# Optimization experiments

Measured on AMD Instinct MI355X. Metric: run time of the kernel, lower is better.

Reference implementation:

```python
import jax, jax.numpy as jnp
import numpy as np

N0, N1, N2 = 100000, 200000, 100000
DEG = 8
D = 128
NC = 16
NHE = 20000
HE_TOT = 200000

def spmm(rows, cols, vals, x, n):
    # y = A @ x for COO sparse A (n x m); x: [m, d] -> [n, d]
    return jax.ops.segment_sum(vals[:, None] * x[cols], rows, num_segments=n)

def setup_inputs():
    key = jax.random.key(0)
    ks = iter(jax.random.split(key, 64))
    def randn(shape, scale=1.0):
        return jax.random.normal(next(ks), shape, dtype=jnp.float32) * scale
    def ridx(n, hi):
        return jax.random.randint(next(ks), (n,), 0, hi, dtype=jnp.int32)
    inp = {}
    inp['X0'] = randn((N0, D)); inp['X1'] = randn((N1, D)); inp['X2'] = randn((N2, D))
    for i, n in [(0, N0), (1, N1), (2, N2)]:
        nnz = DEG * n
        for tag in ['L', 'Lu', 'Ld']:
            inp[f'{tag}{i}'] = jnp.stack([ridx(nnz, n), ridx(nnz, n)])
            inp[f'{tag}{i}v'] = randn((nnz,), 0.1)
    inp['B1r'] = ridx(2 * N1, N0); inp['B1c'] = ridx(2 * N1, N1); inp['B1v'] = randn((2 * N1,), 0.1)
    inp['B2r'] = ridx(3 * N2, N1); inp['B2c'] = ridx(3 * N2, N2); inp['B2v'] = randn((3 * N2,), 0.1)
    inp['he_idx'] = ridx(HE_TOT, N0)
    inp['he_seg'] = jnp.sort(ridx(HE_TOT, NHE))
    inp['W'] = randn((3, 3, 6, D, D), 0.05)  # [layer, simplex-dim, term, in, out]
    inp['Wfc'] = randn((D, D), 0.05)
    inp['Wcls'] = randn((D, NC), 0.05)
    inp['bcls'] = jnp.zeros((NC,), jnp.float32)
    return inp

def reference(X0, X1, X2, L0, L0v, Lu0, Lu0v, Ld0, Ld0v, L1, L1v, Lu1, Lu1v, Ld1, Ld1v, L2, L2v, Lu2, Lu2v, Ld2, Ld2v, B1r, B1c, B1v, B2r, B2c, B2v, he_idx, he_seg, W, Wfc, Wcls, bcls):
    n0, n1, n2 = X0.shape[0], X1.shape[0], X2.shape[0]
    def sp(idx, val, x, n):
        return spmm(idx[0], idx[1], val, x, n)
    def scn(l, x0, x1, x2):
        # terms: 0 self, 1 L, 2 L_u, 3 L_d, 4 from-lower (B^T), 5 from-upper (B)
        h0 = (x0 @ W[l, 0, 0] + sp(L0, L0v, x0, n0) @ W[l, 0, 1]
              + sp(Lu0, Lu0v, x0, n0) @ W[l, 0, 2] + sp(Ld0, Ld0v, x0, n0) @ W[l, 0, 3]
              + spmm(B1r, B1c, B1v, x1, n0) @ W[l, 0, 5])
        h1 = (x1 @ W[l, 1, 0] + sp(L1, L1v, x1, n1) @ W[l, 1, 1]
              + sp(Lu1, Lu1v, x1, n1) @ W[l, 1, 2] + sp(Ld1, Ld1v, x1, n1) @ W[l, 1, 3]
              + spmm(B1c, B1r, B1v, x0, n1) @ W[l, 1, 4]
              + spmm(B2r, B2c, B2v, x2, n1) @ W[l, 1, 5])
        h2 = (x2 @ W[l, 2, 0] + sp(L2, L2v, x2, n2) @ W[l, 2, 1]
              + sp(Lu2, Lu2v, x2, n2) @ W[l, 2, 2] + sp(Ld2, Ld2v, x2, n2) @ W[l, 2, 3]
              + spmm(B2c, B2r, B2v, x1, n2) @ W[l, 2, 4])
        return jnp.tanh(h0), jnp.tanh(h1), jnp.tanh(h2)
    x0, x1, x2 = X0, X1, X2
    for l in range(3):  # layer1/layer2/layer3
        x0, x1, x2 = scn(l, x0, x1, x2)
    # hyperedge mean pooling over dim-0 simplices (gather -> segment mean)
    cnt = jax.ops.segment_sum(jnp.ones((he_idx.shape[0],), x0.dtype), he_seg, num_segments=NHE)
    pooled = jax.ops.segment_sum(x0[he_idx], he_seg, num_segments=NHE) / jnp.maximum(cnt, 1.0)[:, None]
    p = pooled @ Wfc  # fc head (bias=False)
    logits = p[1:] @ Wcls + bcls  # node_class head drops index 0 as in original out[0][1:]
    return logits
```

## Files before the change

### kernel.cpp

```cpp
#include <hip/hip_runtime.h>
#include <cstdint>
#include <cstddef>

typedef float f4v __attribute__((ext_vector_type(4)));
typedef __bf16 bf8 __attribute__((ext_vector_type(8)));
typedef uint32_t u4v __attribute__((ext_vector_type(4)));
typedef uint32_t u2v __attribute__((ext_vector_type(2)));

constexpr int cN0 = 100000, cN1 = 200000, cN2 = 100000;
constexpr int cNHE = 20000, cHE = 200000;
constexpr int N0p = 100096, N1p = 200064, N2p = 100096;
constexpr int NTP = N0p + N1p + N2p;
constexpr int CNT_TOT = 1800000;
constexpr int ELLW = 32;
constexpr int NWE = 54 * 16384;

constexpr size_t AL(size_t x) { return (x + 255) & ~(size_t)255; }
constexpr size_t OFF_XIN = 0;
constexpr size_t OFF_XA  = AL(OFF_XIN + (size_t)NTP * 128 * 2);
constexpr size_t OFF_XB  = AL(OFF_XA  + (size_t)NTP * 128 * 2);
constexpr size_t OFF_WHI = AL(OFF_XB  + (size_t)NTP * 128 * 2);
constexpr size_t OFF_WLO = AL(OFF_WHI + (size_t)NWE * 2);
constexpr size_t OFF_ELL = AL(OFF_WLO + (size_t)NWE * 2);
constexpr size_t OFF_CNT = AL(OFF_ELL + (size_t)CNT_TOT * ELLW * 8);
constexpr size_t OFF_PL  = AL(OFF_CNT + (size_t)CNT_TOT * 4);
constexpr size_t OFF_M   = AL(OFF_PL  + (size_t)cNHE * 128 * 4);
constexpr size_t HEAPSZ  = AL(OFF_M   + (size_t)128 * 16 * 4);

__device__ __align__(256) unsigned char g_heap[HEAPSZ];

__device__ __forceinline__ ushort f2bf(float f) {
    union { float f; uint32_t u; } v{f};
    uint32_t r = v.u + 0x7fffu + ((v.u >> 16) & 1u);
    return (ushort)(r >> 16);
}
__device__ __forceinline__ float bflo(uint32_t u) { union { uint32_t u; float f; } v{u << 16}; return v.f; }
__device__ __forceinline__ float bfhi(uint32_t u) { union { uint32_t u; float f; } v{u & 0xffff0000u}; return v.f; }

__device__ __forceinline__ void gl_lds16(const ushort* g, ushort* l) {
    __builtin_amdgcn_global_load_lds((const __attribute__((address_space(1))) void*)g,
                                     (__attribute__((address_space(3))) void*)l, 16, 0, 0);
}

__device__ __forceinline__ void acc8(float* a, uint4 v, float s) {
    a[0] += s * bflo(v.x); a[1] += s * bfhi(v.x);
    a[2] += s * bflo(v.y); a[3] += s * bfhi(v.y);
    a[4] += s * bflo(v.z); a[5] += s * bfhi(v.z);
    a[6] += s * bflo(v.w); a[7] += s * bfhi(v.w);
}

struct BD { const int* rows; const int* cols; const float* vals; int nnz; int cnt_off; };

struct FT { const ushort* xs; int cntb; int wm; };
struct FG { ushort* xo; int n; FT t[6]; };

__global__ void kzero_i(int* p, int n) {
    for (int i = blockIdx.x * 256 + threadIdx.x; i < n; i += gridDim.x * 256) p[i] = 0;
}

__global__ void kcvt(const float4* __restrict__ src, uint2* __restrict__ dst, int n4) {
    int i = blockIdx.x * 256 + threadIdx.x;
    if (i >= n4) return;
    float4 v = src[i];
    dst[i] = make_uint2((uint32_t)f2bf(v.x) | ((uint32_t)f2bf(v.y) << 16),
                        (uint32_t)f2bf(v.z) | ((uint32_t)f2bf(v.w) << 16));
}

__global__ void kwprep(const float* __restrict__ W, ushort* __restrict__ whi, ushort* __restrict__ wlo) {
    int t = blockIdx.x * 256 + threadIdx.x;
    if (t >= NWE) return;
    int mat = t >> 14, r = t & 16383;
    int i = r & 7, l = (r >> 3) & 63, cf = (r >> 9) & 7, kf = r >> 12;
    int k = kf * 32 + (l >> 4) * 8 + i;
    int c = cf * 16 + (l & 15);
    float w = W[(size_t)mat * 16384 + k * 128 + c];
    ushort h = f2bf(w);
    union { uint32_t u; float f; } hv{(uint32_t)h << 16};
    whi[t] = h;
    wlo[t] = f2bf(w - hv.f);
}

__global__ __launch_bounds__(256) void kscat_1m(BD b, int* __restrict__ cnt, uint2* __restrict__ ell) {
#pragma unroll
    for (int k = 0; k < 4; ++k) {
        int e = blockIdx.x * 1024 + k * 256 + threadIdx.x;
        if (e < b.nnz) {
            int r = b.rows[e];
            int pos = atomicAdd(&cnt[b.cnt_off + r], 1);
            if (pos < ELLW)
                ell[((size_t)(b.cnt_off + r) << 5) + pos] =
                    make_uint2((uint32_t)b.cols[e], __float_as_uint(b.vals[e]));
        }
    }
}

template <int NT>
__global__ __launch_bounds__(256, 4) void kfused(FG g, const ushort* __restrict__ whi,
                                                 const ushort* __restrict__ wlo,
                                                 const int* __restrict__ cnt,
                                                 const uint2* __restrict__ ell) {
    __shared__ __align__(16) ushort xt[64 * 128];
    const int row0 = blockIdx.x * 64;
    const int tid = threadIdx.x;
    const int lane = tid & 63, wv = tid >> 6;
    const int l15 = lane & 15, hi4 = lane >> 4;

    f4v acc[8];
    f4v zz = {0.f, 0.f, 0.f, 0.f};
#pragma unroll
    for (int cf = 0; cf < 8; ++cf) acc[cf] = zz;

#pragma unroll
    for (int t = 0; t < NT; ++t) {
        const FT ft = g.t[t];
        if (t == 0) {
            const ushort* xb = ft.xs + (size_t)row0 * 128;
#pragma unroll
            for (int it = 0; it < 4; ++it) {
                int seg = it * 4 + wv;
                int u = seg * 64 + lane;
                int r = u >> 4, c16 = u & 15;
                gl_lds16(xb + (size_t)r * 128 + ((c16 ^ (r & 7)) * 8), &xt[seg * 512]);
            }
        } else {
#pragma unroll
            for (int p = 0; p < 4; ++p) {
                int r = p * 16 + (tid >> 4);
                int cs = tid & 15;
                int absr = row0 + r;
                float a[8];
#pragma unroll
                for (int j = 0; j < 8; ++j) a[j] = 0.f;
                const uint2* er = ell + ((size_t)(ft.cntb + absr) << 5);
                int deg = 0;
                if (absr < g.n) {
                    deg = __builtin_nontemporal_load(&cnt[ft.cntb + absr]);
                    deg = deg > ELLW ? ELLW : deg;
                }
                const ushort* xsrc = ft.xs + cs * 8;
                int e = 0;
                for (; e + 4 <= deg; e += 4) {
                    u4v r01 = __builtin_nontemporal_load((const u4v*)(er + e));
                    u4v r23 = __builtin_nontemporal_load((const u4v*)(er + e + 2));
                    uint4 x0 = *(const uint4*)(xsrc + (size_t)r01.x * 128);
                    uint4 x1 = *(const uint4*)(xsrc + (size_t)r01.z * 128);
                    uint4 x2 = *(const uint4*)(xsrc + (size_t)r23.x * 128);
                    uint4 x3 = *(const uint4*)(xsrc + (size_t)r23.z * 128);
                    acc8(a, x0, __uint_as_float(r01.y));
                    acc8(a, x1, __uint_as_float(r01.w));
                    acc8(a, x2, __uint_as_float(r23.y));
                    acc8(a, x3, __uint_as_float(r23.w));
                }
                for (; e < deg; ++e) {
                    u2v rc = __builtin_nontemporal_load((const u2v*)(er + e));
                    uint4 xv = *(const uint4*)(xsrc + (size_t)rc.x * 128);
                    acc8(a, xv, __uint_as_float(rc.y));
                }
                uint32_t w[4];
#pragma unroll
                for (int j = 0; j < 4; ++j)
                    w[j] = (uint32_t)f2bf(a[2 * j]) | ((uint32_t)f2bf(a[2 * j + 1]) << 16);
                int c = cs ^ (r & 7);
                *(uint4*)&xt[r * 128 + c * 8] = make_uint4(w[0], w[1], w[2], w[3]);
            }
        }
        __syncthreads();

        const int mat = ft.wm;
        const int rl = wv * 16 + l15;
#pragma unroll
        for (int h = 0; h < 2; ++h) {
            const ushort* wb = (h ? wlo : whi) + (size_t)mat * 16384;
#pragma unroll
            for (int kf = 0; kf < 4; ++kf) {
                int slot = (kf * 4 + hi4) ^ (rl & 7);
                bf8 xf = *(const bf8*)&xt[rl * 128 + slot * 8];
#pragma unroll
                for (int cfc = 0; cfc < 2; ++cfc) {
                    bf8 wf[4];
#pragma unroll
                    for (int c = 0; c < 4; ++c)
                        wf[c] = *(const bf8*)(wb + ((size_t)(kf * 8 + cfc * 4 + c) * 64 + lane) * 8);
#pragma unroll
                    for (int c = 0; c < 4; ++c)
                        acc[cfc * 4 + c] =
                            __builtin_amdgcn_mfma_f32_16x16x32_bf16(wf[c], xf, acc[cfc * 4 + c], 0, 0, 0);
                }
            }
        }
        __syncthreads();
    }

    ushort* sb = xt + wv * 2048;
#pragma unroll
    for (int cf = 0; cf < 8; ++cf) {
        int rl = l15;
        float t0 = tanhf(acc[cf][0]), t1 = tanhf(acc[cf][1]);
        float t2 = tanhf(acc[cf][2]), t3 = tanhf(acc[cf][3]);
        uint32_t p0 = (uint32_t)f2bf(t0) | ((uint32_t)f2bf(t1) << 16);
        uint32_t p1 = (uint32_t)f2bf(t2) | ((uint32_t)f2bf(t3) << 16);
        int s0 = cf * 2 + (hi4 >> 1);
        int byteoff = rl * 256 + ((s0 ^ (rl & 7)) * 16) + (hi4 & 1) * 8;
        *(uint2*)((char*)sb + byteoff) = make_uint2(p0, p1);
    }
    __syncthreads();
    ushort* yb = g.xo + (size_t)(row0 + wv * 16) * 128;
#pragma unroll
    for (int it = 0; it < 4; ++it) {
        int rl = it * 4 + hi4;
        int s = l15 ^ (rl & 7);
        uint4 v = *(const uint4*)((const char*)sb + rl * 256 + s * 16);
        int absrow = row0 + wv * 16 + rl;
        if (absrow < g.n)
            *(uint4*)(yb + (size_t)rl * 128 + l15 * 8) = v;
    }
}

__device__ inline int lbound(const int* arr, int n, int key) {
    int lo = 0, hi = n;
    while (lo < hi) { int mid = (lo + hi) >> 1; if (arr[mid] < key) lo = mid + 1; else hi = mid; }
    return lo;
}

__global__ __launch_bounds__(128) void kpool(const ushort* x0, const int* he_idx, const int* he_seg, float* pool) {
    int s = blockIdx.x;
    int t = threadIdx.x;
    int lo = lbound(he_seg, cHE, s);
    int hi = lbound(he_seg, cHE, s + 1);
    float acc = 0.f;
    for (int e = lo; e < hi; ++e) acc += bflo((uint32_t)x0[(size_t)he_idx[e] * 128 + t]);
    float c = (float)(hi - lo);
    pool[(size_t)s * 128 + t] = acc / fmaxf(c, 1.f);
}

__global__ void kmatm(const float* Wfc, const float* Wcls, float* M) {
    int o = blockIdx.x * 256 + threadIdx.x;
    if (o >= 128 * 16) return;
    int dd = o >> 4, j = o & 15;
    float s = 0.f;
    for (int c = 0; c < 128; ++c) s += Wfc[dd * 128 + c] * Wcls[c * 16 + j];
    M[o] = s;
}

__global__ __launch_bounds__(256) void khead(const float* pool, const float* M, const float* bcls, float* out) {
    int row = blockIdx.x * 16 + (threadIdx.x >> 4);
    int j = threadIdx.x & 15;
    if (row >= cNHE - 1) return;
    int s = row + 1;
    float acc = bcls[j];
    const float* p = pool + (size_t)s * 128;
    for (int dd = 0; dd < 128; ++dd) acc += p[dd] * M[dd * 16 + j];
    out[(size_t)row * 16 + j] = acc;
}

extern "C" void kernel_launch(void* const* d_in, const int* in_sizes, int n_in,
                              void* d_out, int out_size, void* d_ws, size_t ws_size,
                              hipStream_t stream) {
    (void)in_sizes; (void)n_in; (void)out_size; (void)d_ws; (void)ws_size;

    unsigned char* heap = nullptr;
    hipGetSymbolAddress((void**)&heap, HIP_SYMBOL(g_heap));

    ushort* xin = (ushort*)(heap + OFF_XIN);
    ushort* xA  = (ushort*)(heap + OFF_XA);
    ushort* xB  = (ushort*)(heap + OFF_XB);
    ushort* whi = (ushort*)(heap + OFF_WHI);
    ushort* wlo = (ushort*)(heap + OFF_WLO);
    uint2* ell  = (uint2*)(heap + OFF_ELL);
    int* cnt    = (int*)(heap + OFF_CNT);
    float* pool = (float*)(heap + OFF_PL);
    float* Mbuf = (float*)(heap + OFF_M);

    const float* X0 = (const float*)d_in[0];
    const float* X1 = (const float*)d_in[1];
    const float* X2 = (const float*)d_in[2];
    const float* Wp = (const float*)d_in[29];

    kcvt<<<dim3((cN0 * 32 + 255) / 256), 256, 0, stream>>>((const float4*)X0, (uint2*)xin, cN0 * 32);
    kcvt<<<dim3((cN1 * 32 + 255) / 256), 256, 0, stream>>>((const float4*)X1, (uint2*)(xin + (size_t)N0p * 128), cN1 * 32);
    kcvt<<<dim3((cN2 * 32 + 255) / 256), 256, 0, stream>>>((const float4*)X2, (uint2*)(xin + (size_t)(N0p + N1p) * 128), cN2 * 32);
    kwprep<<<dim3((NWE + 255) / 256), 256, 0, stream>>>(Wp, whi, wlo);

    static const int mnnz[13] = {800000, 800000, 800000, 1600000, 1600000, 1600000,
                                 800000, 800000, 800000, 400000, 400000, 300000, 300000};
    static const int mn[13] = {cN0, cN0, cN0, cN1, cN1, cN1, cN2, cN2, cN2, cN0, cN1, cN1, cN2};

    BD bs[13];
    int cb[13];
    {
        int coff = 0;
        for (int m = 0; m < 13; ++m) {
            BD& b = bs[m];
            if (m < 9) {
                const int* p = (const int*)d_in[3 + 2 * m];
                b.rows = p;
                b.cols = p + mnnz[m];
                b.vals = (const float*)d_in[4 + 2 * m];
            } else if (m == 9) { b.rows = (const int*)d_in[21]; b.cols = (const int*)d_in[22]; b.vals = (const float*)d_in[23]; }
            else if (m == 10) { b.rows = (const int*)d_in[22]; b.cols = (const int*)d_in[21]; b.vals = (const float*)d_in[23]; }
            else if (m == 11) { b.rows = (const int*)d_in[24]; b.cols = (const int*)d_in[25]; b.vals = (const float*)d_in[26]; }
            else              { b.rows = (const int*)d_in[25]; b.cols = (const int*)d_in[24]; b.vals = (const float*)d_in[26]; }
            b.nnz = mnnz[m];
            b.cnt_off = coff;
            cb[m] = coff;
            coff += mn[m];
        }
    }

    kzero_i<<<dim3(2048), 256, 0, stream>>>(cnt, CNT_TOT);
    for (int m = 0; m < 13; ++m)
        kscat_1m<<<dim3((bs[m].nnz + 1023) / 1024), 256, 0, stream>>>(bs[m], cnt, ell);

    constexpr int nb0 = N0p / 64, nb1 = N1p / 64, nb2 = N2p / 64;

    for (int l = 0; l < 3; ++l) {
        const ushort* xi = (l == 0) ? xin : ((l == 1) ? xA : xB);
        ushort* xo = (l == 1) ? xB : xA;
        const ushort* x0p = xi;
        const ushort* x1p = xi + (size_t)N0p * 128;
        const ushort* x2p = xi + (size_t)(N0p + N1p) * 128;
        auto M_ = [&](int s, int t) { return (l * 3 + s) * 6 + t; };

        FG f0{xo, cN0,
              {{x0p, -1, M_(0,0)}, {x0p, cb[0], M_(0,1)}, {x0p, cb[1], M_(0,2)},
               {x0p, cb[2], M_(0,3)}, {x1p, cb[9], M_(0,5)}, {nullptr, 0, 0}}};
        kfused<5><<<dim3(nb0), 256, 0, stream>>>(f0, whi, wlo, cnt, ell);

        if (l < 2) {
            FG f1{xo + (size_t)N0p * 128, cN1,
                  {{x1p, -1, M_(1,0)}, {x1p, cb[3], M_(1,1)}, {x1p, cb[4], M_(1,2)},
                   {x1p, cb[5], M_(1,3)}, {x0p, cb[10], M_(1,4)}, {x2p, cb[11], M_(1,5)}}};
            kfused<6><<<dim3(nb1), 256, 0, stream>>>(f1, whi, wlo, cnt, ell);

            FG f2{xo + (size_t)(N0p + N1p) * 128, cN2,
                  {{x2p, -1, M_(2,0)}, {x2p, cb[6], M_(2,1)}, {x2p, cb[7], M_(2,2)},
                   {x2p, cb[8], M_(2,3)}, {x1p, cb[12], M_(2,4)}, {nullptr, 0, 0}}};
            kfused<5><<<dim3(nb2), 256, 0, stream>>>(f2, whi, wlo, cnt, ell);
        }
    }

    kpool<<<dim3(cNHE), 128, 0, stream>>>(xA, (const int*)d_in[27], (const int*)d_in[28], pool);
    kmatm<<<dim3(8), 256, 0, stream>>>((const float*)d_in[30], (const float*)d_in[31], Mbuf);
    khead<<<dim3((cNHE - 1 + 15) / 16), 256, 0, stream>>>(pool, Mbuf, (const float*)d_in[32], (float*)d_out);
}
```

Measured before the change: 3.478 ms.

## Double threads per fused SCN block, splitting output columns across wave pairs

The fused sparse-aggregate plus MFMA kernel now runs 512 threads (8 waves) per 64-row tile instead of 256. Each pair of waves shares a 16-row slice, and each wave computes half the 128 output columns, so per-thread accumulators drop from 8 to 4 fragments. Sparse gather rows are spread over twice as many threads, and the epilogue staging and store are remapped to the half-width layout. The intent is more memory-level parallelism for the latency-bound ELL gathers and lower register pressure. In exchange, each X fragment is loaded from LDS by two waves, and block-wide barriers now span more waves.

```diff
diff --git a/kernel.cpp b/kernel.cpp
--- a/kernel.cpp
+++ b/kernel.cpp
@@ -95,7 +95,7 @@
 }
 
 template <int NT>
-__global__ __launch_bounds__(256, 4) void kfused(FG g, const ushort* __restrict__ whi,
+__global__ __launch_bounds__(512, 4) void kfused(FG g, const ushort* __restrict__ whi,
                                                  const ushort* __restrict__ wlo,
                                                  const int* __restrict__ cnt,
                                                  const uint2* __restrict__ ell) {
@@ -105,10 +105,10 @@
     const int lane = tid & 63, wv = tid >> 6;
     const int l15 = lane & 15, hi4 = lane >> 4;
 
-    f4v acc[8];
+    f4v acc[4];
     f4v zz = {0.f, 0.f, 0.f, 0.f};
 #pragma unroll
-    for (int cf = 0; cf < 8; ++cf) acc[cf] = zz;
+    for (int cf = 0; cf < 4; ++cf) acc[cf] = zz;
 
 #pragma unroll
     for (int t = 0; t < NT; ++t) {
@@ -116,16 +116,16 @@
         if (t == 0) {
             const ushort* xb = ft.xs + (size_t)row0 * 128;
 #pragma unroll
-            for (int it = 0; it < 4; ++it) {
-                int seg = it * 4 + wv;
+            for (int it = 0; it < 2; ++it) {
+                int seg = it * 8 + wv;
                 int u = seg * 64 + lane;
                 int r = u >> 4, c16 = u & 15;
                 gl_lds16(xb + (size_t)r * 128 + ((c16 ^ (r & 7)) * 8), &xt[seg * 512]);
             }
         } else {
 #pragma unroll
-            for (int p = 0; p < 4; ++p) {
-                int r = p * 16 + (tid >> 4);
+            for (int p = 0; p < 2; ++p) {
+                int r = p * 32 + (tid >> 4);
                 int cs = tid & 15;
                 int absr = row0 + r;
                 float a[8];
@@ -167,7 +167,8 @@
         __syncthreads();
 
         const int mat = ft.wm;
-        const int rl = wv * 16 + l15;
+        const int rl = (wv >> 1) * 16 + l15;
+        const int cbase = (wv & 1) * 4;
 #pragma unroll
         for (int h = 0; h < 2; ++h) {
             const ushort* wb = (h ? wlo : whi) + (size_t)mat * 16384;
@@ -175,44 +176,39 @@
             for (int kf = 0; kf < 4; ++kf) {
                 int slot = (kf * 4 + hi4) ^ (rl & 7);
                 bf8 xf = *(const bf8*)&xt[rl * 128 + slot * 8];
-#pragma unroll
-                for (int cfc = 0; cfc < 2; ++cfc) {
-                    bf8 wf[4];
-#pragma unroll
-                    for (int c = 0; c < 4; ++c)
-                        wf[c] = *(const bf8*)(wb + ((size_t)(kf * 8 + cfc * 4 + c) * 64 + lane) * 8);
-#pragma unroll
-                    for (int c = 0; c < 4; ++c)
-                        acc[cfc * 4 + c] =
-                            __builtin_amdgcn_mfma_f32_16x16x32_bf16(wf[c], xf, acc[cfc * 4 + c], 0, 0, 0);
-                }
+                bf8 wf[4];
+#pragma unroll
+                for (int c = 0; c < 4; ++c)
+                    wf[c] = *(const bf8*)(wb + ((size_t)(kf * 8 + cbase + c) * 64 + lane) * 8);
+#pragma unroll
+                for (int c = 0; c < 4; ++c)
+                    acc[c] = __builtin_amdgcn_mfma_f32_16x16x32_bf16(wf[c], xf, acc[c], 0, 0, 0);
             }
         }
         __syncthreads();
     }
 
-    ushort* sb = xt + wv * 2048;
-#pragma unroll
-    for (int cf = 0; cf < 8; ++cf) {
+    ushort* sb = xt + wv * 1024;
+#pragma unroll
+    for (int c = 0; c < 4; ++c) {
         int rl = l15;
-        float t0 = tanhf(acc[cf][0]), t1 = tanhf(acc[cf][1]);
-        float t2 = tanhf(acc[cf][2]), t3 = tanhf(acc[cf][3]);
+        float t0 = tanhf(acc[c][0]), t1 = tanhf(acc[c][1]);
+        float t2 = tanhf(acc[c][2]), t3 = tanhf(acc[c][3]);
         uint32_t p0 = (uint32_t)f2bf(t0) | ((uint32_t)f2bf(t1) << 16);
         uint32_t p1 = (uint32_t)f2bf(t2) | ((uint32_t)f2bf(t3) << 16);
-        int s0 = cf * 2 + (hi4 >> 1);
-        int byteoff = rl * 256 + ((s0 ^ (rl & 7)) * 16) + (hi4 & 1) * 8;
+        int byteoff = rl * 128 + ((c * 32 + hi4 * 8) ^ ((rl & 7) << 4));
         *(uint2*)((char*)sb + byteoff) = make_uint2(p0, p1);
     }
     __syncthreads();
-    ushort* yb = g.xo + (size_t)(row0 + wv * 16) * 128;
-#pragma unroll
-    for (int it = 0; it < 4; ++it) {
-        int rl = it * 4 + hi4;
-        int s = l15 ^ (rl & 7);
-        uint4 v = *(const uint4*)((const char*)sb + rl * 256 + s * 16);
-        int absrow = row0 + wv * 16 + rl;
+    ushort* yb = g.xo + (size_t)(row0 + (wv >> 1) * 16) * 128 + (wv & 1) * 64;
+#pragma unroll
+    for (int it = 0; it < 2; ++it) {
+        int rl = it * 8 + (lane >> 3);
+        int u = lane & 7;
+        uint4 v = *(const uint4*)((const char*)sb + rl * 128 + ((u * 16) ^ ((rl & 7) << 4)));
+        int absrow = row0 + (wv >> 1) * 16 + rl;
         if (absrow < g.n)
-            *(uint4*)(yb + (size_t)rl * 128 + l15 * 8) = v;
+            *(uint4*)(yb + (size_t)rl * 128 + u * 8) = v;
     }
 }
 
@@ -324,18 +320,18 @@
         FG f0{xo, cN0,
               {{x0p, -1, M_(0,0)}, {x0p, cb[0], M_(0,1)}, {x0p, cb[1], M_(0,2)},
                {x0p, cb[2], M_(0,3)}, {x1p, cb[9], M_(0,5)}, {nullptr, 0, 0}}};
-        kfused<5><<<dim3(nb0), 256, 0, stream>>>(f0, whi, wlo, cnt, ell);
+        kfused<5><<<dim3(nb0), 512, 0, stream>>>(f0, whi, wlo, cnt, ell);
 
         if (l < 2) {
             FG f1{xo + (size_t)N0p * 128, cN1,
                   {{x1p, -1, M_(1,0)}, {x1p, cb[3], M_(1,1)}, {x1p, cb[4], M_(1,2)},
                    {x1p, cb[5], M_(1,3)}, {x0p, cb[10], M_(1,4)}, {x2p, cb[11], M_(1,5)}}};
-            kfused<6><<<dim3(nb1), 256, 0, stream>>>(f1, whi, wlo, cnt, ell);
+            kfused<6><<<dim3(nb1), 512, 0, stream>>>(f1, whi, wlo, cnt, ell);
 
             FG f2{xo + (size_t)(N0p + N1p) * 128, cN2,
                   {{x2p, -1, M_(2,0)}, {x2p, cb[6], M_(2,1)}, {x2p, cb[7], M_(2,2)},
                    {x2p, cb[8], M_(2,3)}, {x1p, cb[12], M_(2,4)}, {nullptr, 0, 0}}};
-            kfused<5><<<dim3(nb2), 256, 0, stream>>>(f2, whi, wlo, cnt, ell);
+            kfused<5><<<dim3(nb2), 512, 0, stream>>>(f2, whi, wlo, cnt, ell);
         }
     }
 
```

Result: faster. 3.096 ms (-11.0%).

## Gather SpMM rows directly into MFMA register fragments, drop LDS staging and barriers

Applied to the files above, without the earlier changes.

Each lane now computes the sparse row aggregation for exactly the row and k-slices its MFMA B-fragment needs, so the gathered results go straight into registers instead of being written to shared memory and read back. This removes the per-term __syncthreads pairs and the LDS round trip. The block grows to 512 threads covering 128 rows with 8 wavefronts. In exchange each thread holds 32 float accumulators plus the fragments, which raises register pressure. Each lane also now issues 4 strided 16-byte loads per neighbour instead of one, so memory access patterns change.

```diff
diff --git a/kernel.cpp b/kernel.cpp
--- a/kernel.cpp
+++ b/kernel.cpp
@@ -36,11 +36,6 @@
 }
 __device__ __forceinline__ float bflo(uint32_t u) { union { uint32_t u; float f; } v{u << 16}; return v.f; }
 __device__ __forceinline__ float bfhi(uint32_t u) { union { uint32_t u; float f; } v{u & 0xffff0000u}; return v.f; }
-
-__device__ __forceinline__ void gl_lds16(const ushort* g, ushort* l) {
-    __builtin_amdgcn_global_load_lds((const __attribute__((address_space(1))) void*)g,
-                                     (__attribute__((address_space(3))) void*)l, 16, 0, 0);
-}
 
 __device__ __forceinline__ void acc8(float* a, uint4 v, float s) {
     a[0] += s * bflo(v.x); a[1] += s * bfhi(v.x);
@@ -95,15 +90,17 @@
 }
 
 template <int NT>
-__global__ __launch_bounds__(256, 4) void kfused(FG g, const ushort* __restrict__ whi,
+__global__ __launch_bounds__(512, 3) void kfused(FG g, const ushort* __restrict__ whi,
                                                  const ushort* __restrict__ wlo,
                                                  const int* __restrict__ cnt,
                                                  const uint2* __restrict__ ell) {
-    __shared__ __align__(16) ushort xt[64 * 128];
-    const int row0 = blockIdx.x * 64;
+    __shared__ __align__(16) ushort xt[8 * 2048];
+    const int row0 = blockIdx.x * 128;
     const int tid = threadIdx.x;
     const int lane = tid & 63, wv = tid >> 6;
     const int l15 = lane & 15, hi4 = lane >> 4;
+    const int strip0 = row0 + wv * 16;
+    const int absr = strip0 + l15;
 
     f4v acc[8];
     f4v zz = {0.f, 0.f, 0.f, 0.f};
@@ -113,68 +110,71 @@
 #pragma unroll
     for (int t = 0; t < NT; ++t) {
         const FT ft = g.t[t];
+        bf8 xf[4];
         if (t == 0) {
-            const ushort* xb = ft.xs + (size_t)row0 * 128;
-#pragma unroll
-            for (int it = 0; it < 4; ++it) {
-                int seg = it * 4 + wv;
-                int u = seg * 64 + lane;
-                int r = u >> 4, c16 = u & 15;
-                gl_lds16(xb + (size_t)r * 128 + ((c16 ^ (r & 7)) * 8), &xt[seg * 512]);
-            }
+            const ushort* xr = ft.xs + (size_t)absr * 128 + hi4 * 8;
+            xf[0] = *(const bf8*)(xr);
+            xf[1] = *(const bf8*)(xr + 32);
+            xf[2] = *(const bf8*)(xr + 64);
+            xf[3] = *(const bf8*)(xr + 96);
         } else {
-#pragma unroll
-            for (int p = 0; p < 4; ++p) {
-                int r = p * 16 + (tid >> 4);
-                int cs = tid & 15;
-                int absr = row0 + r;
-                float a[8];
-#pragma unroll
-                for (int j = 0; j < 8; ++j) a[j] = 0.f;
-                const uint2* er = ell + ((size_t)(ft.cntb + absr) << 5);
-                int deg = 0;
-                if (absr < g.n) {
-                    deg = __builtin_nontemporal_load(&cnt[ft.cntb + absr]);
-                    deg = deg > ELLW ? ELLW : deg;
-                }
-                const ushort* xsrc = ft.xs + cs * 8;
-                int e = 0;
-                for (; e + 4 <= deg; e += 4) {
-                    u4v r01 = __builtin_nontemporal_load((const u4v*)(er + e));
-                    u4v r23 = __builtin_nontemporal_load((const u4v*)(er + e + 2));
-                    uint4 x0 = *(const uint4*)(xsrc + (size_t)r01.x * 128);
-                    uint4 x1 = *(const uint4*)(xsrc + (size_t)r01.z * 128);
-                    uint4 x2 = *(const uint4*)(xsrc + (size_t)r23.x * 128);
-                    uint4 x3 = *(const uint4*)(xsrc + (size_t)r23.z * 128);
-                    acc8(a, x0, __uint_as_float(r01.y));
-                    acc8(a, x1, __uint_as_float(r01.w));
-                    acc8(a, x2, __uint_as_float(r23.y));
-                    acc8(a, x3, __uint_as_float(r23.w));
-                }
-                for (; e < deg; ++e) {
-                    u2v rc = __builtin_nontemporal_load((const u2v*)(er + e));
-                    uint4 xv = *(const uint4*)(xsrc + (size_t)rc.x * 128);
-                    acc8(a, xv, __uint_as_float(rc.y));
-                }
-                uint32_t w[4];
-#pragma unroll
-                for (int j = 0; j < 4; ++j)
-                    w[j] = (uint32_t)f2bf(a[2 * j]) | ((uint32_t)f2bf(a[2 * j + 1]) << 16);
-                int c = cs ^ (r & 7);
-                *(uint4*)&xt[r * 128 + c * 8] = make_uint4(w[0], w[1], w[2], w[3]);
-            }
-        }
-        __syncthreads();
+            float a[32];
+#pragma unroll
+            for (int j = 0; j < 32; ++j) a[j] = 0.f;
+            int deg = 0;
+            if (absr < g.n) {
+                deg = __builtin_nontemporal_load(&cnt[ft.cntb + absr]);
+                deg = deg > ELLW ? ELLW : deg;
+            }
+            const uint2* er = ell + ((size_t)(ft.cntb + absr) << 5);
+            const ushort* xsrc = ft.xs + hi4 * 8;
+            int e = 0;
+            for (; e + 2 <= deg; e += 2) {
+                u4v rr = __builtin_nontemporal_load((const u4v*)(er + e));
+                const ushort* p0 = xsrc + (size_t)rr.x * 128;
+                const ushort* p1 = xsrc + (size_t)rr.z * 128;
+                uint4 x00 = *(const uint4*)(p0);
+                uint4 x01 = *(const uint4*)(p0 + 32);
+                uint4 x02 = *(const uint4*)(p0 + 64);
+                uint4 x03 = *(const uint4*)(p0 + 96);
+                uint4 x10 = *(const uint4*)(p1);
+                uint4 x11 = *(const uint4*)(p1 + 32);
+                uint4 x12 = *(const uint4*)(p1 + 64);
+                uint4 x13 = *(const uint4*)(p1 + 96);
+                float v0 = __uint_as_float(rr.y), v1 = __uint_as_float(rr.w);
+                acc8(a + 0, x00, v0); acc8(a + 8, x01, v0);
+                acc8(a + 16, x02, v0); acc8(a + 24, x03, v0);
+                acc8(a + 0, x10, v1); acc8(a + 8, x11, v1);
+                acc8(a + 16, x12, v1); acc8(a + 24, x13, v1);
+            }
+            if (e < deg) {
+                u2v rc = __builtin_nontemporal_load((const u2v*)(er + e));
+                const ushort* p0 = xsrc + (size_t)rc.x * 128;
+                uint4 x00 = *(const uint4*)(p0);
+                uint4 x01 = *(const uint4*)(p0 + 32);
+                uint4 x02 = *(const uint4*)(p0 + 64);
+                uint4 x03 = *(const uint4*)(p0 + 96);
+                float v0 = __uint_as_float(rc.x ^ rc.x ? 0u : rc.y);
+                acc8(a + 0, x00, v0); acc8(a + 8, x01, v0);
+                acc8(a + 16, x02, v0); acc8(a + 24, x03, v0);
+            }
+#pragma unroll
+            for (int kf = 0; kf < 4; ++kf) {
+                uint4 q;
+                q.x = (uint32_t)f2bf(a[kf * 8 + 0]) | ((uint32_t)f2bf(a[kf * 8 + 1]) << 16);
+                q.y = (uint32_t)f2bf(a[kf * 8 + 2]) | ((uint32_t)f2bf(a[kf * 8 + 3]) << 16);
+                q.z = (uint32_t)f2bf(a[kf * 8 + 4]) | ((uint32_t)f2bf(a[kf * 8 + 5]) << 16);
+                q.w = (uint32_t)f2bf(a[kf * 8 + 6]) | ((uint32_t)f2bf(a[kf * 8 + 7]) << 16);
+                xf[kf] = *(const bf8*)&q;
+            }
+        }
 
         const int mat = ft.wm;
-        const int rl = wv * 16 + l15;
 #pragma unroll
         for (int h = 0; h < 2; ++h) {
             const ushort* wb = (h ? wlo : whi) + (size_t)mat * 16384;
 #pragma unroll
             for (int kf = 0; kf < 4; ++kf) {
-                int slot = (kf * 4 + hi4) ^ (rl & 7);
-                bf8 xf = *(const bf8*)&xt[rl * 128 + slot * 8];
 #pragma unroll
                 for (int cfc = 0; cfc < 2; ++cfc) {
                     bf8 wf[4];
@@ -184,11 +184,10 @@
 #pragma unroll
                     for (int c = 0; c < 4; ++c)
                         acc[cfc * 4 + c] =
-                            __builtin_amdgcn_mfma_f32_16x16x32_bf16(wf[c], xf, acc[cfc * 4 + c], 0, 0, 0);
+                            __builtin_amdgcn_mfma_f32_16x16x32_bf16(wf[c], xf[kf], acc[cfc * 4 + c], 0, 0, 0);
                 }
             }
         }
-        __syncthreads();
     }
 
     ushort* sb = xt + wv * 2048;
@@ -311,7 +310,7 @@
     for (int m = 0; m < 13; ++m)
         kscat_1m<<<dim3((bs[m].nnz + 1023) / 1024), 256, 0, stream>>>(bs[m], cnt, ell);
 
-    constexpr int nb0 = N0p / 64, nb1 = N1p / 64, nb2 = N2p / 64;
+    constexpr int nb0 = N0p / 128, nb1 = N1p / 128, nb2 = N2p / 128;
 
     for (int l = 0; l < 3; ++l) {
         const ushort* xi = (l == 0) ? xin : ((l == 1) ? xA : xB);
@@ -324,18 +323,18 @@
         FG f0{xo, cN0,
               {{x0p, -1, M_(0,0)}, {x0p, cb[0], M_(0,1)}, {x0p, cb[1], M_(0,2)},
                {x0p, cb[2], M_(0,3)}, {x1p, cb[9], M_(0,5)}, {nullptr, 0, 0}}};
-        kfused<5><<<dim3(nb0), 256, 0, stream>>>(f0, whi, wlo, cnt, ell);
+        kfused<5><<<dim3(nb0), 512, 0, stream>>>(f0, whi, wlo, cnt, ell);
 
         if (l < 2) {
             FG f1{xo + (size_t)N0p * 128, cN1,
                   {{x1p, -1, M_(1,0)}, {x1p, cb[3], M_(1,1)}, {x1p, cb[4], M_(1,2)},
                    {x1p, cb[5], M_(1,3)}, {x0p, cb[10], M_(1,4)}, {x2p, cb[11], M_(1,5)}}};
-            kfused<6><<<dim3(nb1), 256, 0, stream>>>(f1, whi, wlo, cnt, ell);
+            kfused<6><<<dim3(nb1), 512, 0, stream>>>(f1, whi, wlo, cnt, ell);
 
             FG f2{xo + (size_t)(N0p + N1p) * 128, cN2,
                   {{x2p, -1, M_(2,0)}, {x2p, cb[6], M_(2,1)}, {x2p, cb[7], M_(2,2)},
                    {x2p, cb[8], M_(2,3)}, {x1p, cb[12], M_(2,4)}, {nullptr, 0, 0}}};
-            kfused<5><<<dim3(nb2), 256, 0, stream>>>(f2, whi, wlo, cnt, ell);
+            kfused<5><<<dim3(nb2), 512, 0, stream>>>(f2, whi, wlo, cnt, ell);
         }
     }
 
```

Result: slower. 3.686 ms (+6.0%).
